# Kernel tuning notes

Hardware: AMD Instinct MI355X
Metric: run time of the kernel (lower is better)

Reference implementation:

```python
import jax, jax.numpy as jnp
import numpy as np

B, L, WD = 4096, 30, 300          # batch of news, title length, word dim
H, AD = 20, 20                    # attention heads, per-head dim
MD = H * AD                       # multi_dim = 400
E, ED = 10, 100                   # entities per news, entity dim
QD = 200                          # query_vector_dim
CAT, CD = 18, 50                  # category vocab / dim
SUB, SD = 300, 50                 # subcategory vocab / dim


def _mha(x, wq, bq, wk, bk, wv, bv):
    # x: [B, L, Din] -> [B, L, MD]; standard multi-head self-attention
    b, l, _ = x.shape
    q = (x @ wq + bq).reshape(b, l, H, AD)
    k = (x @ wk + bk).reshape(b, l, H, AD)
    v = (x @ wv + bv).reshape(b, l, H, AD)
    scores = jnp.einsum('blhd,bmhd->bhlm', q, k) / jnp.sqrt(jnp.asarray(AD, x.dtype))
    attn = jax.nn.softmax(scores, axis=-1)
    out = jnp.einsum('bhlm,bmhd->blhd', attn, v)
    return out.reshape(b, l, MD)


def _layernorm(x, g, b):
    mu = jnp.mean(x, axis=-1, keepdims=True)
    var = jnp.var(x, axis=-1, keepdims=True)
    return (x - mu) / jnp.sqrt(var + 1e-5) * g + b


def _additive(x, w, b, q):
    # x: [B, L, D] -> [B, D]
    scores = jnp.tanh(x @ w + b) @ q            # [B, L]
    alpha = jax.nn.softmax(scores, axis=-1)
    return jnp.einsum('bl,bld->bd', alpha, x)


def setup_inputs() -> dict:
    key = jax.random.key(0)
    ks = iter(jax.random.split(key, 40))
    n = lambda shape, s=0.02: (jax.random.normal(next(ks), shape, dtype=jnp.float32) * s)
    inp = {
        'word_embedding': jax.random.normal(next(ks), (B, L, WD), dtype=jnp.float32),
        'entity_embedding': jax.random.normal(next(ks), (B, E, ED), dtype=jnp.float32),
        'category_index': jax.random.randint(next(ks), (B,), 0, CAT, dtype=jnp.int64 if jax.config.jax_enable_x64 else jnp.int32),
        'subcategory_index': jax.random.randint(next(ks), (B,), 0, SUB, dtype=jnp.int64 if jax.config.jax_enable_x64 else jnp.int32),
        # category / subcategory branches
        'emb_cat': n((CAT, CD), 1.0), 'fc1_w': n((CD, MD)), 'fc1_b': jnp.zeros((MD,), jnp.float32),
        'emb_sub': n((SUB, SD), 1.0), 'fc2_w': n((SD, MD)), 'fc2_b': jnp.zeros((MD,), jnp.float32),
        # word multi-head self-attention
        'wq': n((WD, MD)), 'bq': jnp.zeros((MD,), jnp.float32),
        'wk': n((WD, MD)), 'bk': jnp.zeros((MD,), jnp.float32),
        'wv': n((WD, MD)), 'bv': jnp.zeros((MD,), jnp.float32),
        # shared LayerNorm
        'ln_g': jnp.ones((MD,), jnp.float32), 'ln_b': jnp.zeros((MD,), jnp.float32),
        # word additive attention
        'wa_w': n((MD, QD)), 'wa_b': jnp.zeros((QD,), jnp.float32), 'wa_q': n((QD,), 1.0),
        # entity branch: fc3 + GCN (learnable adjacency over the E entities of a news)
        'fc3_w': n((ED, ED)), 'fc3_b': jnp.zeros((ED,), jnp.float32),
        'gcn_A': n((E, E), 1.0), 'gcn_w': n((ED, MD)), 'gcn_b': jnp.zeros((MD,), jnp.float32),
        'ea_w': n((MD, QD)), 'ea_b': jnp.zeros((QD,), jnp.float32), 'ea_q': n((QD,), 1.0),
        # final news-level additive attention over 4 views
        'na_w': n((MD, QD)), 'na_b': jnp.zeros((QD,), jnp.float32), 'na_q': n((QD,), 1.0),
    }
    return inp


def reference(word_embedding, entity_embedding, category_index, subcategory_index,
              emb_cat, fc1_w, fc1_b, emb_sub, fc2_w, fc2_b,
              wq, bq, wk, bk, wv, bv, ln_g, ln_b,
              wa_w, wa_b, wa_q, fc3_w, fc3_b, gcn_A, gcn_w, gcn_b,
              ea_w, ea_b, ea_q, na_w, na_b, na_q):
    # category / subcategory reps (dropout is identity in eval)
    cat_rep = jnp.tanh(emb_cat[category_index] @ fc1_w + fc1_b)      # [B, MD]
    sub_rep = jnp.tanh(emb_sub[subcategory_index] @ fc2_w + fc2_b)   # [B, MD]
    # word branch
    w = _mha(word_embedding, wq, bq, wk, bk, wv, bv)                 # [B, L, MD]
    w = _layernorm(w, ln_g, ln_b)
    word_rep = jnp.tanh(_additive(w, wa_w, wa_b, wa_q))              # [B, MD]
    # entity branch: fc3 -> intra-news GCN -> shared LayerNorm
    e = jnp.tanh(entity_embedding @ fc3_w + fc3_b)                   # [B, E, ED]
    e = jax.nn.relu(jnp.einsum('ef,bfd->bed', gcn_A, e) @ gcn_w + gcn_b)  # [B, E, MD]
    e = _layernorm(e, ln_g, ln_b)
    ent_rep = jnp.tanh(_additive(e, ea_w, ea_b, ea_q))               # [B, MD]
    # fuse the 4 views with additive attention
    views = jnp.stack([word_rep, ent_rep, cat_rep, sub_rep], axis=1)  # [B, 4, MD]
    news_rep = jnp.tanh(_additive(views, na_w, na_b, na_q))          # [B, MD]
    return news_rep
```

## Files before the change

kernel.cpp:

```cpp
#include <hip/hip_runtime.h>
#include <hip/hip_bf16.h>
#include <math.h>

#define B_  4096
#define L_  30
#define WD_ 300
#define H_  20
#define AD_ 20
#define MD_ 400
#define E_  10
#define ED_ 100
#define QD_ 200
#define CD_ 50
#define SD_ 50

typedef unsigned short ushort_t;
typedef __attribute__((ext_vector_type(8))) short bf16x8_t;
typedef __attribute__((ext_vector_type(4))) float f32x4_t;

#define SX_STR   328
#define QKVQ_STR 306
#define SOB_STR  408
#define OUTB_STR 424
#define SOUT_STR 401
#define P_STR    40
#define WT_K     320
#define WAT_K    416

#define N_WT    (1200 * WT_K)
#define N_WAT   (208 * WAT_K)
#define N_FC3T  (112 * 128)
#define N_GCNT  (400 * 128)
#define N_EAT   (208 * WAT_K)

union FragU {
  unsigned  u[4];
  short     s[8];
  bf16x8_t  h;
};

__device__ __forceinline__ ushort_t f2bf(float f) {
  unsigned u = __builtin_bit_cast(unsigned, f);
  unsigned r = (u + 0x7fffu + ((u >> 16) & 1u)) >> 16;
  return (ushort_t)r;
}
__device__ __forceinline__ float bf2f(ushort_t h) {
  return __builtin_bit_cast(float, ((unsigned)h) << 16);
}
__device__ __forceinline__ float wave_reduce_sum(float v) {
  #pragma unroll
  for (int off = 32; off > 0; off >>= 1) v += __shfl_xor(v, off);
  return v;
}
__device__ __forceinline__ void split2(float v, ushort_t* __restrict__ H,
                                       ushort_t* __restrict__ Lo, int idx) {
  const ushort_t h = f2bf(v);
  H[idx] = h;
  Lo[idx] = f2bf(v - bf2f(h));
}

__global__ __launch_bounds__(256) void prep_weights(
    const float* __restrict__ wq, const float* __restrict__ wk, const float* __restrict__ wv,
    const float* __restrict__ wa_w, const float* __restrict__ fc3_w,
    const float* __restrict__ gcn_w, const float* __restrict__ ea_w,
    ushort_t* __restrict__ Wt, ushort_t* __restrict__ Wat,
    ushort_t* __restrict__ fc3TH, ushort_t* __restrict__ fc3TL,
    ushort_t* __restrict__ gcnTH, ushort_t* __restrict__ gcnTL,
    ushort_t* __restrict__ eaTH, ushort_t* __restrict__ eaTL)
{
  int idx = blockIdx.x * 256 + threadIdx.x;
  if (idx < N_WT) {
    const int n = idx / WT_K, k = idx - n * WT_K;
    float v = 0.f;
    if (k < WD_) {
      const float* w = (n < 400) ? wq : (n < 800) ? wk : wv;
      const int c = (n < 400) ? n : (n < 800) ? n - 400 : n - 800;
      v = w[k * MD_ + c];
    }
    Wt[idx] = f2bf(v);
    return;
  }
  idx -= N_WT;
  if (idx < N_WAT) {
    const int q = idx / WAT_K, d = idx - q * WAT_K;
    Wat[idx] = (q < QD_ && d < MD_) ? f2bf(wa_w[d * QD_ + q]) : (ushort_t)0;
    return;
  }
  idx -= N_WAT;
  if (idx < N_FC3T) {
    const int n = idx / 128, k = idx - n * 128;
    const float v = (n < ED_ && k < ED_) ? fc3_w[k * ED_ + n] : 0.f;
    split2(v, fc3TH, fc3TL, idx);
    return;
  }
  idx -= N_FC3T;
  if (idx < N_GCNT) {
    const int n = idx / 128, k = idx - n * 128;
    const float v = (k < ED_) ? gcn_w[k * MD_ + n] : 0.f;
    split2(v, gcnTH, gcnTL, idx);
    return;
  }
  idx -= N_GCNT;
  if (idx < N_EAT) {
    const int q = idx / WAT_K, d = idx - q * WAT_K;
    const float v = (q < QD_ && d < MD_) ? ea_w[d * QD_ + q] : 0.f;
    split2(v, eaTH, eaTL, idx);
  }
}

__global__ __launch_bounds__(512, 4) void word_branch_kernel(
    const float* __restrict__ X,
    const ushort_t* __restrict__ Wt, const ushort_t* __restrict__ Wat,
    const float* __restrict__ bq, const float* __restrict__ bk, const float* __restrict__ bv,
    const float* __restrict__ ln_g, const float* __restrict__ ln_b,
    const float* __restrict__ wa_b, const float* __restrict__ wa_q,
    float* __restrict__ word_rep)
{
  __shared__ __align__(16) ushort_t sX[32 * SX_STR];
  __shared__ __align__(16) ushort_t qkvQ[30 * QKVQ_STR];
  __shared__ __align__(16) ushort_t sOb[30 * SOB_STR];
  __shared__ __align__(16) ushort_t pT[8 * 16 * P_STR];
  __shared__ float sSc[32];
  __shared__ float sAlpha[32];

  const int b    = blockIdx.x;
  const int tid  = threadIdx.x;
  const int wave = tid >> 6;
  const int lane = tid & 63;
  const int lr   = lane & 15;
  const int kg   = lane >> 4;

  const float* xb = X + (size_t)b * (L_ * WD_);
  for (int idx = tid; idx < 32 * 320; idx += 512) {
    const int r = idx / 320, c = idx - (idx / 320) * 320;
    const float v = (r < L_ && c < WD_) ? xb[r * WD_ + c] : 0.f;
    sX[r * SX_STR + c] = f2bf(v);
  }
  for (int id = tid; id < 30 * 8; id += 512) {
    const int r = id >> 3, c = 400 + (id & 7);
    sOb[r * SOB_STR + c] = 0;
  }
  if (tid < 32) sSc[tid] = 0.f;
  __syncthreads();

  ushort_t* pw = &pT[wave * (16 * P_STR)];
  #pragma unroll 1
  for (int pass = 0; pass < 4; ++pass) {
    const int qb = (100 * pass) & ~15;
    const int p100 = 100 * pass;

    for (int t = wave; t < 21; t += 8) {
      const int sect = t / 7, ti = t - sect * 7;
      const int gq = qb + ti * 16 + lr;
      const int gcol = gq + ((sect == 0) ? 0 : (sect == 1) ? 400 : 800);
      const ushort_t* wbase = &Wt[gcol * WT_K + kg * 8];
      f32x4_t acc0 = {0,0,0,0}, acc1 = {0,0,0,0};
      #pragma unroll
      for (int ks = 0; ks < 10; ++ks) {
        bf16x8_t bf  = *reinterpret_cast<const bf16x8_t*>(wbase + ks * 32);
        bf16x8_t af0 = *reinterpret_cast<const bf16x8_t*>(&sX[lr * SX_STR + ks * 32 + kg * 8]);
        bf16x8_t af1 = *reinterpret_cast<const bf16x8_t*>(&sX[(16 + lr) * SX_STR + ks * 32 + kg * 8]);
        acc0 = __builtin_amdgcn_mfma_f32_16x16x32_bf16(af0, bf, acc0, 0, 0, 0);
        acc1 = __builtin_amdgcn_mfma_f32_16x16x32_bf16(af1, bf, acc1, 0, 0, 0);
      }
      const float bias = (gcol < 400) ? bq[gcol] : (gcol < 800) ? bk[gcol - 400] : bv[gcol - 800];
      const int lq = gq - p100;
      if (lq >= 0 && lq < 100) {
        const int lcol = sect * 102 + lq;
        #pragma unroll
        for (int i = 0; i < 4; ++i) {
          qkvQ[(kg * 4 + i) * QKVQ_STR + lcol] = f2bf(acc0[i] + bias);
          const int r2 = 16 + kg * 4 + i;
          if (r2 < L_) qkvQ[r2 * QKVQ_STR + lcol] = f2bf(acc1[i] + bias);
        }
      }
    }
    __syncthreads();

    for (int u = wave; u < 10; u += 8) {
      const int hl = u >> 1, mt = u & 1;
      const int h = pass * 5 + hl;
      const int qloc = hl * 20, kloc = 102 + hl * 20, vloc = 204 + hl * 20;

      bf16x8_t aq, bkf[2];
      {
        FragU fq;
        fq.u[0]=fq.u[1]=fq.u[2]=fq.u[3]=0;
        const bool okrow = (mt == 0) || (lr < 14);
        if (okrow && kg < 3) {
          const ushort_t* pq = &qkvQ[(mt * 16 + lr) * QKVQ_STR + qloc + kg * 8];
          fq.u[0] = *(const unsigned*)(pq);     fq.u[1] = *(const unsigned*)(pq + 2);
          if (kg < 2) { fq.u[2] = *(const unsigned*)(pq + 4); fq.u[3] = *(const unsigned*)(pq + 6); }
        }
        aq = fq.h;
      }
      #pragma unroll
      for (int t = 0; t < 2; ++t) {
        FragU fk;
        fk.u[0]=fk.u[1]=fk.u[2]=fk.u[3]=0;
        const bool okrow = (t == 0) || (lr < 14);
        if (okrow && kg < 3) {
          const ushort_t* pk = &qkvQ[(t * 16 + lr) * QKVQ_STR + kloc + kg * 8];
          fk.u[0] = *(const unsigned*)(pk);     fk.u[1] = *(const unsigned*)(pk + 2);
          if (kg < 2) { fk.u[2] = *(const unsigned*)(pk + 4); fk.u[3] = *(const unsigned*)(pk + 6); }
        }
        bkf[t] = fk.h;
      }
      f32x4_t c0 = {0,0,0,0}, c1 = {0,0,0,0};
      c0 = __builtin_amdgcn_mfma_f32_16x16x32_bf16(aq, bkf[0], c0, 0, 0, 0);
      c1 = __builtin_amdgcn_mfma_f32_16x16x32_bf16(aq, bkf[1], c1, 0, 0, 0);

      const float SCALE = 0.2236067977499790f;
      #pragma unroll
      for (int i = 0; i < 4; ++i) {
        const float v0 = c0[i] * SCALE;
        const float v1 = (lr < 14) ? c1[i] * SCALE : -1e30f;
        float mx = fmaxf(v0, v1);
        mx = fmaxf(mx, __shfl_xor(mx, 1));
        mx = fmaxf(mx, __shfl_xor(mx, 2));
        mx = fmaxf(mx, __shfl_xor(mx, 4));
        mx = fmaxf(mx, __shfl_xor(mx, 8));
        const float e0 = __expf(v0 - mx);
        const float e1 = (lr < 14) ? __expf(v1 - mx) : 0.f;
        float s = e0 + e1;
        s += __shfl_xor(s, 1);
        s += __shfl_xor(s, 2);
        s += __shfl_xor(s, 4);
        s += __shfl_xor(s, 8);
        const float inv = 1.f / s;
        const int row = kg * 4 + i;
        pw[row * P_STR + lr]      = f2bf(e0 * inv);
        pw[row * P_STR + 16 + lr] = f2bf(e1 * inv);
      }
      __asm__ volatile("s_waitcnt lgkmcnt(0)" ::: "memory");

      bf16x8_t ap = *reinterpret_cast<const bf16x8_t*>(&pw[lr * P_STR + kg * 8]);
      bf16x8_t bvf[2];
      #pragma unroll
      for (int nt = 0; nt < 2; ++nt) {
        FragU f;
        const int d = nt * 16 + lr;
        if (d < AD_) {
          #pragma unroll
          for (int j = 0; j < 8; ++j) {
            const int rm = kg * 8 + j;
            f.s[j] = (rm < L_) ? (short)qkvQ[rm * QKVQ_STR + vloc + d] : (short)0;
          }
        } else {
          f.u[0]=f.u[1]=f.u[2]=f.u[3]=0;
        }
        bvf[nt] = f.h;
      }
      f32x4_t o0 = {0,0,0,0}, o1 = {0,0,0,0};
      o0 = __builtin_amdgcn_mfma_f32_16x16x32_bf16(ap, bvf[0], o0, 0, 0, 0);
      o1 = __builtin_amdgcn_mfma_f32_16x16x32_bf16(ap, bvf[1], o1, 0, 0, 0);

      #pragma unroll
      for (int nt = 0; nt < 2; ++nt) {
        const f32x4_t o = nt ? o1 : o0;
        const int d = nt * 16 + lr;
        if (d < AD_) {
          #pragma unroll
          for (int i = 0; i < 4; ++i) {
            const int r = mt * 16 + kg * 4 + i;
            if (r < L_) sOb[r * SOB_STR + h * AD_ + d] = f2bf(o[i]);
          }
        }
      }
    }
    __syncthreads();
  }

  for (int r = wave; r < L_; r += 8) {
    float s = 0.f, s2 = 0.f;
    #pragma unroll
    for (int j = 0; j < 7; ++j) {
      const int d = lane + j * 64;
      if (d < MD_) { const float v = bf2f(sOb[r * SOB_STR + d]); s += v; s2 += v * v; }
    }
    s  = wave_reduce_sum(s);
    s2 = wave_reduce_sum(s2);
    const float mu  = s * (1.f / MD_);
    const float var = s2 * (1.f / MD_) - mu * mu;
    const float inv = rsqrtf(var + 1e-5f);
    #pragma unroll
    for (int j = 0; j < 7; ++j) {
      const int d = lane + j * 64;
      if (d < MD_) {
        const float nv = (bf2f(sOb[r * SOB_STR + d]) - mu) * inv * ln_g[d] + ln_b[d];
        sOb[r * SOB_STR + d] = f2bf(nv);
      }
    }
  }
  __syncthreads();

  for (int t = wave; t < 26; t += 8) {
    const int mt = t & 1, nt = t >> 1;
    const int row = mt * 16 + lr;
    const bool okrow = row < L_;
    const ushort_t* wbase = &Wat[(nt * 16 + lr) * WAT_K + kg * 8];
    f32x4_t acc = {0,0,0,0};
    #pragma unroll
    for (int ks = 0; ks < 13; ++ks) {
      bf16x8_t af;
      if (okrow && !(ks == 12 && kg == 3)) {
        af = *reinterpret_cast<const bf16x8_t*>(&sOb[row * SOB_STR + ks * 32 + kg * 8]);
      } else {
        FragU z; z.u[0]=z.u[1]=z.u[2]=z.u[3]=0; af = z.h;
      }
      bf16x8_t wf = *reinterpret_cast<const bf16x8_t*>(wbase + ks * 32);
      acc = __builtin_amdgcn_mfma_f32_16x16x32_bf16(af, wf, acc, 0, 0, 0);
    }
    const int q = nt * 16 + lr;
    if (q < QD_) {
      const float bb = wa_b[q], qq = wa_q[q];
      #pragma unroll
      for (int i = 0; i < 4; ++i) {
        const int rr = mt * 16 + kg * 4 + i;
        if (rr < L_) atomicAdd(&sSc[rr], tanhf(acc[i] + bb) * qq);
      }
    }
  }
  __syncthreads();

  if (wave == 0) {
    const float v = (lane < L_) ? sSc[lane] : -1e30f;
    float mx = v;
    #pragma unroll
    for (int off = 32; off > 0; off >>= 1) mx = fmaxf(mx, __shfl_xor(mx, off));
    const float e = (lane < L_) ? __expf(v - mx) : 0.f;
    float s = e;
    #pragma unroll
    for (int off = 32; off > 0; off >>= 1) s += __shfl_xor(s, off);
    if (lane < L_) sAlpha[lane] = e / s;
  }
  __syncthreads();

  if (tid < MD_) {
    const int d = tid;
    float acc = 0.f;
    #pragma unroll 6
    for (int l = 0; l < L_; ++l) acc += sAlpha[l] * bf2f(sOb[l * SOB_STR + d]);
    word_rep[(size_t)b * MD_ + d] = tanhf(acc);
  }
}

__global__ __launch_bounds__(512, 4) void entity_branch_kernel(
    const float* __restrict__ Ein,
    const ushort_t* __restrict__ fc3TH, const ushort_t* __restrict__ fc3TL,
    const float* __restrict__ fc3_b,
    const float* __restrict__ gcn_A,
    const ushort_t* __restrict__ gcnTH, const ushort_t* __restrict__ gcnTL,
    const float* __restrict__ gcn_b,
    const float* __restrict__ ln_g, const float* __restrict__ ln_b,
    const ushort_t* __restrict__ eaTH, const ushort_t* __restrict__ eaTL,
    const float* __restrict__ ea_b, const float* __restrict__ ea_q,
    float* __restrict__ ent_rep)
{
  __shared__ __align__(16) ushort_t sEh[16 * 136], sEl[16 * 136];
  __shared__ __align__(16) float    eF[E_ * 104];
  __shared__ __align__(16) ushort_t gH[16 * 136], gL[16 * 136];
  __shared__ __align__(16) float    sR[16 * SOUT_STR];
  __shared__ __align__(16) ushort_t oH[16 * OUTB_STR], oL[16 * OUTB_STR];
  __shared__ float sSc[16];
  __shared__ float sAlpha[16];

  const int b    = blockIdx.x;
  const int tid  = threadIdx.x;
  const int wave = tid >> 6;
  const int lane = tid & 63;
  const int lr   = lane & 15;
  const int kg   = lane >> 4;

  for (int id = tid; id < 16 * 128; id += 512) {
    const int r = id >> 7, c = id & 127;
    const float v = (r < E_ && c < ED_) ? Ein[(size_t)b * (E_ * ED_) + r * ED_ + c] : 0.f;
    const ushort_t hh = f2bf(v);
    sEh[r * 136 + c] = hh;
    sEl[r * 136 + c] = f2bf(v - bf2f(hh));
  }
  for (int id = tid; id < 16 * 136; id += 512) { gH[id] = 0; gL[id] = 0; }
  for (int id = tid; id < 16 * OUTB_STR; id += 512) { oH[id] = 0; oL[id] = 0; }
  if (tid < 16) sSc[tid] = 0.f;
  __syncthreads();

  for (int nt = wave; nt < 7; nt += 8) {
    f32x4_t acc = {0,0,0,0};
    #pragma unroll
    for (int ks = 0; ks < 4; ++ks) {
      const int kb = ks * 32 + kg * 8;
      bf16x8_t ah = *reinterpret_cast<const bf16x8_t*>(&sEh[lr * 136 + kb]);
      bf16x8_t al = *reinterpret_cast<const bf16x8_t*>(&sEl[lr * 136 + kb]);
      bf16x8_t wh = *reinterpret_cast<const bf16x8_t*>(&fc3TH[(nt * 16 + lr) * 128 + kb]);
      bf16x8_t wl = *reinterpret_cast<const bf16x8_t*>(&fc3TL[(nt * 16 + lr) * 128 + kb]);
      acc = __builtin_amdgcn_mfma_f32_16x16x32_bf16(ah, wh, acc, 0, 0, 0);
      acc = __builtin_amdgcn_mfma_f32_16x16x32_bf16(al, wh, acc, 0, 0, 0);
      acc = __builtin_amdgcn_mfma_f32_16x16x32_bf16(ah, wl, acc, 0, 0, 0);
    }
    const int d = nt * 16 + lr;
    if (d < ED_) {
      const float bias = fc3_b[d];
      #pragma unroll
      for (int i = 0; i < 4; ++i) {
        const int r = kg * 4 + i;
        if (r < E_) eF[r * 104 + d] = tanhf(acc[i] + bias);
      }
    }
  }
  __syncthreads();

  for (int id = tid; id < E_ * ED_; id += 512) {
    const int i = id / ED_, d = id - (id / ED_) * ED_;
    float acc = 0.f;
    #pragma unroll
    for (int f = 0; f < E_; ++f) acc += gcn_A[i * E_ + f] * eF[f * 104 + d];
    const ushort_t hh = f2bf(acc);
    gH[i * 136 + d] = hh;
    gL[i * 136 + d] = f2bf(acc - bf2f(hh));
  }
  __syncthreads();

  for (int nt = wave; nt < 25; nt += 8) {
    f32x4_t acc = {0,0,0,0};
    #pragma unroll
    for (int ks = 0; ks < 4; ++ks) {
      const int kb = ks * 32 + kg * 8;
      bf16x8_t ah = *reinterpret_cast<const bf16x8_t*>(&gH[lr * 136 + kb]);
      bf16x8_t al = *reinterpret_cast<const bf16x8_t*>(&gL[lr * 136 + kb]);
      bf16x8_t wh = *reinterpret_cast<const bf16x8_t*>(&gcnTH[(nt * 16 + lr) * 128 + kb]);
      bf16x8_t wl = *reinterpret_cast<const bf16x8_t*>(&gcnTL[(nt * 16 + lr) * 128 + kb]);
      acc = __builtin_amdgcn_mfma_f32_16x16x32_bf16(ah, wh, acc, 0, 0, 0);
      acc = __builtin_amdgcn_mfma_f32_16x16x32_bf16(al, wh, acc, 0, 0, 0);
      acc = __builtin_amdgcn_mfma_f32_16x16x32_bf16(ah, wl, acc, 0, 0, 0);
    }
    const int d = nt * 16 + lr;
    const float bias = gcn_b[d];
    #pragma unroll
    for (int i = 0; i < 4; ++i) {
      const int r = kg * 4 + i;
      if (r < E_) sR[r * SOUT_STR + d] = fmaxf(acc[i] + bias, 0.f);
    }
  }
  __syncthreads();

  for (int r = wave; r < E_; r += 8) {
    float s = 0.f, s2 = 0.f;
    for (int d = lane; d < MD_; d += 64) { const float v = sR[r * SOUT_STR + d]; s += v; s2 += v * v; }
    s  = wave_reduce_sum(s);
    s2 = wave_reduce_sum(s2);
    const float mu  = s * (1.f / MD_);
    const float var = s2 * (1.f / MD_) - mu * mu;
    const float inv = rsqrtf(var + 1e-5f);
    for (int d = lane; d < MD_; d += 64) {
      const float nv = (sR[r * SOUT_STR + d] - mu) * inv * ln_g[d] + ln_b[d];
      sR[r * SOUT_STR + d] = nv;
      const ushort_t hh = f2bf(nv);
      oH[r * OUTB_STR + d] = hh;
      oL[r * OUTB_STR + d] = f2bf(nv - bf2f(hh));
    }
  }
  __syncthreads();

  for (int nt = wave; nt < 13; nt += 8) {
    f32x4_t acc = {0,0,0,0};
    for (int ks = 0; ks < 13; ++ks) {
      const int kb = ks * 32 + kg * 8;
      bf16x8_t ah = *reinterpret_cast<const bf16x8_t*>(&oH[lr * OUTB_STR + kb]);
      bf16x8_t al = *reinterpret_cast<const bf16x8_t*>(&oL[lr * OUTB_STR + kb]);
      bf16x8_t wh = *reinterpret_cast<const bf16x8_t*>(&eaTH[(nt * 16 + lr) * WAT_K + kb]);
      bf16x8_t wl = *reinterpret_cast<const bf16x8_t*>(&eaTL[(nt * 16 + lr) * WAT_K + kb]);
      acc = __builtin_amdgcn_mfma_f32_16x16x32_bf16(ah, wh, acc, 0, 0, 0);
      acc = __builtin_amdgcn_mfma_f32_16x16x32_bf16(al, wh, acc, 0, 0, 0);
      acc = __builtin_amdgcn_mfma_f32_16x16x32_bf16(ah, wl, acc, 0, 0, 0);
    }
    const int q = nt * 16 + lr;
    if (q < QD_) {
      const float bb = ea_b[q], qq = ea_q[q];
      #pragma unroll
      for (int i = 0; i < 4; ++i) {
        const int r = kg * 4 + i;
        if (r < E_) atomicAdd(&sSc[r], tanhf(acc[i] + bb) * qq);
      }
    }
  }
  __syncthreads();

  if (wave == 0) {
    const float v = (lane < E_) ? sSc[lane] : -1e30f;
    float mx = v;
    #pragma unroll
    for (int off = 32; off > 0; off >>= 1) mx = fmaxf(mx, __shfl_xor(mx, off));
    const float e = (lane < E_) ? __expf(v - mx) : 0.f;
    float s = e;
    #pragma unroll
    for (int off = 32; off > 0; off >>= 1) s += __shfl_xor(s, off);
    if (lane < E_) sAlpha[lane] = e / s;
  }
  __syncthreads();

  if (tid < MD_) {
    const int d = tid;
    float acc = 0.f;
    #pragma unroll
    for (int i = 0; i < E_; ++i) acc += sAlpha[i] * sR[i * SOUT_STR + d];
    ent_rep[(size_t)b * MD_ + d] = tanhf(acc);
  }
}

__global__ __launch_bounds__(256) void catsub_kernel(
    const int* __restrict__ cat_idx, const int* __restrict__ sub_idx,
    const float* __restrict__ emb_cat, const float* __restrict__ fc1_w, const float* __restrict__ fc1_b,
    const float* __restrict__ emb_sub, const float* __restrict__ fc2_w, const float* __restrict__ fc2_b,
    float* __restrict__ cat_rep, float* __restrict__ sub_rep)
{
  int idx = blockIdx.x * 256 + threadIdx.x;
  const int total = B_ * MD_;
  if (idx < total) {
    const int b = idx / MD_, d = idx - (idx / MD_) * MD_;
    const float* row = emb_cat + (size_t)cat_idx[b] * CD_;
    float acc = fc1_b[d];
    #pragma unroll
    for (int k = 0; k < CD_; ++k) acc += row[k] * fc1_w[k * MD_ + d];
    cat_rep[idx] = tanhf(acc);
  } else {
    idx -= total;
    if (idx < total) {
      const int b = idx / MD_, d = idx - (idx / MD_) * MD_;
      const float* row = emb_sub + (size_t)sub_idx[b] * SD_;
      float acc = fc2_b[d];
      #pragma unroll
      for (int k = 0; k < SD_; ++k) acc += row[k] * fc2_w[k * MD_ + d];
      sub_rep[idx] = tanhf(acc);
    }
  }
}

__global__ __launch_bounds__(256) void fuse_kernel(
    const float* __restrict__ word_rep, const float* __restrict__ ent_rep,
    const float* __restrict__ cat_rep, const float* __restrict__ sub_rep,
    const float* __restrict__ na_w, const float* __restrict__ na_b, const float* __restrict__ na_q,
    float* __restrict__ out)
{
  __shared__ float sViews[4][MD_];
  __shared__ float sSc[4];
  __shared__ float sAlpha[4];
  const int b = blockIdx.x, tid = threadIdx.x;
  for (int d = tid; d < MD_; d += 256) {
    sViews[0][d] = word_rep[(size_t)b * MD_ + d];
    sViews[1][d] = ent_rep[(size_t)b * MD_ + d];
    sViews[2][d] = cat_rep[(size_t)b * MD_ + d];
    sViews[3][d] = sub_rep[(size_t)b * MD_ + d];
  }
  if (tid < 4) sSc[tid] = 0.f;
  __syncthreads();
  for (int id = tid; id < 4 * QD_; id += 256) {
    const int v = id / QD_, q = id - (id / QD_) * QD_;
    float acc = na_b[q];
    #pragma unroll 4
    for (int d = 0; d < MD_; ++d) acc += sViews[v][d] * na_w[d * QD_ + q];
    atomicAdd(&sSc[v], tanhf(acc) * na_q[q]);
  }
  __syncthreads();
  if (tid == 0) {
    float mx = -1e30f;
    for (int v = 0; v < 4; ++v) mx = fmaxf(mx, sSc[v]);
    float sum = 0.f;
    for (int v = 0; v < 4; ++v) { const float e = __expf(sSc[v] - mx); sAlpha[v] = e; sum += e; }
    const float inv = 1.f / sum;
    for (int v = 0; v < 4; ++v) sAlpha[v] *= inv;
  }
  __syncthreads();
  for (int d = tid; d < MD_; d += 256) {
    const float acc = sAlpha[0] * sViews[0][d] + sAlpha[1] * sViews[1][d] +
                      sAlpha[2] * sViews[2][d] + sAlpha[3] * sViews[3][d];
    out[(size_t)b * MD_ + d] = tanhf(acc);
  }
}

extern "C" void kernel_launch(void* const* d_in, const int* in_sizes, int n_in,
                              void* d_out, int out_size, void* d_ws, size_t ws_size,
                              hipStream_t stream) {
  const float* X        = (const float*)d_in[0];
  const float* Ein      = (const float*)d_in[1];
  const int*   cat_idx  = (const int*)d_in[2];
  const int*   sub_idx  = (const int*)d_in[3];
  const float* emb_cat  = (const float*)d_in[4];
  const float* fc1_w    = (const float*)d_in[5];
  const float* fc1_b    = (const float*)d_in[6];
  const float* emb_sub  = (const float*)d_in[7];
  const float* fc2_w    = (const float*)d_in[8];
  const float* fc2_b    = (const float*)d_in[9];
  const float* wq       = (const float*)d_in[10];
  const float* bq       = (const float*)d_in[11];
  const float* wk       = (const float*)d_in[12];
  const float* bk       = (const float*)d_in[13];
  const float* wv       = (const float*)d_in[14];
  const float* bv       = (const float*)d_in[15];
  const float* ln_g     = (const float*)d_in[16];
  const float* ln_b     = (const float*)d_in[17];
  const float* wa_w     = (const float*)d_in[18];
  const float* wa_b     = (const float*)d_in[19];
  const float* wa_q     = (const float*)d_in[20];
  const float* fc3_w    = (const float*)d_in[21];
  const float* fc3_b    = (const float*)d_in[22];
  const float* gcn_A    = (const float*)d_in[23];
  const float* gcn_w    = (const float*)d_in[24];
  const float* gcn_b    = (const float*)d_in[25];
  const float* ea_w     = (const float*)d_in[26];
  const float* ea_b     = (const float*)d_in[27];
  const float* ea_q     = (const float*)d_in[28];
  const float* na_w     = (const float*)d_in[29];
  const float* na_b     = (const float*)d_in[30];
  const float* na_q     = (const float*)d_in[31];

  float* out = (float*)d_out;
  const size_t BM = (size_t)B_ * MD_;
  float* word_rep = (float*)d_ws;
  float* ent_rep  = word_rep + BM;
  float* cat_rep  = ent_rep + BM;
  float* sub_rep  = cat_rep + BM;
  ushort_t* Wt    = (ushort_t*)(sub_rep + BM);
  ushort_t* Wat   = Wt + N_WT;
  ushort_t* fc3TH = Wat + N_WAT;
  ushort_t* fc3TL = fc3TH + N_FC3T;
  ushort_t* gcnTH = fc3TL + N_FC3T;
  ushort_t* gcnTL = gcnTH + N_GCNT;
  ushort_t* eaTH  = gcnTL + N_GCNT;
  ushort_t* eaTL  = eaTH + N_EAT;

  {
    const int total = N_WT + N_WAT + N_FC3T + N_GCNT + N_EAT;
    prep_weights<<<(total + 255) / 256, 256, 0, stream>>>(
        wq, wk, wv, wa_w, fc3_w, gcn_w, ea_w,
        Wt, Wat, fc3TH, fc3TL, gcnTH, gcnTL, eaTH, eaTL);
  }
  word_branch_kernel<<<B_, 512, 0, stream>>>(X, Wt, Wat, bq, bk, bv,
                                             ln_g, ln_b, wa_b, wa_q, word_rep);
  entity_branch_kernel<<<B_, 512, 0, stream>>>(Ein, fc3TH, fc3TL, fc3_b, gcn_A,
                                               gcnTH, gcnTL, gcn_b,
                                               ln_g, ln_b, eaTH, eaTL, ea_b, ea_q, ent_rep);
  catsub_kernel<<<(2 * B_ * MD_) / 256, 256, 0, stream>>>(cat_idx, sub_idx,
                                                          emb_cat, fc1_w, fc1_b,
                                                          emb_sub, fc2_w, fc2_b,
                                                          cat_rep, sub_rep);
  fuse_kernel<<<B_, 256, 0, stream>>>(word_rep, ent_rep, cat_rep, sub_rep,
                                      na_w, na_b, na_q, out);
}
```

Before: 1.316 ms.

## Merge word, entity and cat/sub kernels into one interleaved mega-kernel

Combines the word-branch, entity-branch and category/subcategory kernels into a single launch. Blocks alternate between word and entity work, and the cat/sub work comes last, with all three sharing one union shared-memory buffer. The aim is to cut launch gaps and tail effects and to mix the MFMA-heavy word blocks with the lighter entity blocks on each CU so they overlap. In exchange, every block reserves the largest shared-memory footprint, and the cat/sub blocks now reserve about 74KB they do not use. Register pressure is also bounded by the heavier branch, which may hurt occupancy.

```diff
diff --git a/kernel.cpp b/kernel.cpp
--- a/kernel.cpp
+++ b/kernel.cpp
@@ -32,6 +32,8 @@
 #define N_FC3T  (112 * 128)
 #define N_GCNT  (400 * 128)
 #define N_EAT   (208 * WAT_K)
+
+#define SMEM_BYTES 74496
 
 union FragU {
   unsigned  u[4];
@@ -108,7 +110,8 @@
   }
 }
 
-__global__ __launch_bounds__(512, 4) void word_branch_kernel(
+__device__ void word_body(
+    int b, char* smem,
     const float* __restrict__ X,
     const ushort_t* __restrict__ Wt, const ushort_t* __restrict__ Wat,
     const float* __restrict__ bq, const float* __restrict__ bk, const float* __restrict__ bv,
@@ -116,14 +119,13 @@
     const float* __restrict__ wa_b, const float* __restrict__ wa_q,
     float* __restrict__ word_rep)
 {
-  __shared__ __align__(16) ushort_t sX[32 * SX_STR];
-  __shared__ __align__(16) ushort_t qkvQ[30 * QKVQ_STR];
-  __shared__ __align__(16) ushort_t sOb[30 * SOB_STR];
-  __shared__ __align__(16) ushort_t pT[8 * 16 * P_STR];
-  __shared__ float sSc[32];
-  __shared__ float sAlpha[32];
-
-  const int b    = blockIdx.x;
+  ushort_t* sX     = (ushort_t*)(smem + 0);
+  ushort_t* qkvQ   = (ushort_t*)(smem + 20992);
+  ushort_t* sOb    = (ushort_t*)(smem + 39360);
+  ushort_t* pT     = (ushort_t*)(smem + 63840);
+  float*    sSc    = (float*)(smem + 74080);
+  float*    sAlpha = (float*)(smem + 74208);
+
   const int tid  = threadIdx.x;
   const int wave = tid >> 6;
   const int lane = tid & 63;
@@ -143,7 +145,7 @@
   if (tid < 32) sSc[tid] = 0.f;
   __syncthreads();
 
-  ushort_t* pw = &pT[wave * (16 * P_STR)];
+  ushort_t* pw = pT + wave * (16 * P_STR);
   #pragma unroll 1
   for (int pass = 0; pass < 4; ++pass) {
     const int qb = (100 * pass) & ~15;
@@ -345,7 +347,8 @@
   }
 }
 
-__global__ __launch_bounds__(512, 4) void entity_branch_kernel(
+__device__ void entity_body(
+    int b, char* smem,
     const float* __restrict__ Ein,
     const ushort_t* __restrict__ fc3TH, const ushort_t* __restrict__ fc3TL,
     const float* __restrict__ fc3_b,
@@ -357,15 +360,17 @@
     const float* __restrict__ ea_b, const float* __restrict__ ea_q,
     float* __restrict__ ent_rep)
 {
-  __shared__ __align__(16) ushort_t sEh[16 * 136], sEl[16 * 136];
-  __shared__ __align__(16) float    eF[E_ * 104];
-  __shared__ __align__(16) ushort_t gH[16 * 136], gL[16 * 136];
-  __shared__ __align__(16) float    sR[16 * SOUT_STR];
-  __shared__ __align__(16) ushort_t oH[16 * OUTB_STR], oL[16 * OUTB_STR];
-  __shared__ float sSc[16];
-  __shared__ float sAlpha[16];
-
-  const int b    = blockIdx.x;
+  ushort_t* sEh    = (ushort_t*)(smem + 0);
+  ushort_t* sEl    = (ushort_t*)(smem + 4352);
+  float*    eF     = (float*)(smem + 8704);
+  ushort_t* gH     = (ushort_t*)(smem + 12864);
+  ushort_t* gL     = (ushort_t*)(smem + 17216);
+  float*    sR     = (float*)(smem + 21568);
+  ushort_t* oH     = (ushort_t*)(smem + 47232);
+  ushort_t* oL     = (ushort_t*)(smem + 60800);
+  float*    sSc    = (float*)(smem + 74368);
+  float*    sAlpha = (float*)(smem + 74432);
+
   const int tid  = threadIdx.x;
   const int wave = tid >> 6;
   const int lane = tid & 63;
@@ -507,30 +512,57 @@
   }
 }
 
-__global__ __launch_bounds__(256) void catsub_kernel(
+__global__ __launch_bounds__(512, 4) void mega_kernel(
+    const float* __restrict__ X,
+    const ushort_t* __restrict__ Wt, const ushort_t* __restrict__ Wat,
+    const float* __restrict__ bq, const float* __restrict__ bk, const float* __restrict__ bv,
+    const float* __restrict__ ln_g, const float* __restrict__ ln_b,
+    const float* __restrict__ wa_b, const float* __restrict__ wa_q,
+    float* __restrict__ word_rep,
+    const float* __restrict__ Ein,
+    const ushort_t* __restrict__ fc3TH, const ushort_t* __restrict__ fc3TL,
+    const float* __restrict__ fc3_b,
+    const float* __restrict__ gcn_A,
+    const ushort_t* __restrict__ gcnTH, const ushort_t* __restrict__ gcnTL,
+    const float* __restrict__ gcn_b,
+    const ushort_t* __restrict__ eaTH, const ushort_t* __restrict__ eaTL,
+    const float* __restrict__ ea_b, const float* __restrict__ ea_q,
+    float* __restrict__ ent_rep,
     const int* __restrict__ cat_idx, const int* __restrict__ sub_idx,
     const float* __restrict__ emb_cat, const float* __restrict__ fc1_w, const float* __restrict__ fc1_b,
     const float* __restrict__ emb_sub, const float* __restrict__ fc2_w, const float* __restrict__ fc2_b,
     float* __restrict__ cat_rep, float* __restrict__ sub_rep)
 {
-  int idx = blockIdx.x * 256 + threadIdx.x;
-  const int total = B_ * MD_;
-  if (idx < total) {
-    const int b = idx / MD_, d = idx - (idx / MD_) * MD_;
-    const float* row = emb_cat + (size_t)cat_idx[b] * CD_;
-    float acc = fc1_b[d];
-    #pragma unroll
-    for (int k = 0; k < CD_; ++k) acc += row[k] * fc1_w[k * MD_ + d];
-    cat_rep[idx] = tanhf(acc);
+  __shared__ __align__(16) char smem[SMEM_BYTES];
+  const int bid = blockIdx.x;
+  if (bid < 2 * B_) {
+    if ((bid & 1) == 0) {
+      word_body(bid >> 1, smem, X, Wt, Wat, bq, bk, bv, ln_g, ln_b,
+                wa_b, wa_q, word_rep);
+    } else {
+      entity_body(bid >> 1, smem, Ein, fc3TH, fc3TL, fc3_b, gcn_A,
+                  gcnTH, gcnTL, gcn_b, ln_g, ln_b, eaTH, eaTL, ea_b, ea_q, ent_rep);
+    }
   } else {
-    idx -= total;
+    int idx = (bid - 2 * B_) * 512 + threadIdx.x;
+    const int total = B_ * MD_;
     if (idx < total) {
       const int b = idx / MD_, d = idx - (idx / MD_) * MD_;
-      const float* row = emb_sub + (size_t)sub_idx[b] * SD_;
-      float acc = fc2_b[d];
-      #pragma unroll
-      for (int k = 0; k < SD_; ++k) acc += row[k] * fc2_w[k * MD_ + d];
-      sub_rep[idx] = tanhf(acc);
+      const float* row = emb_cat + (size_t)cat_idx[b] * CD_;
+      float acc = fc1_b[d];
+      #pragma unroll
+      for (int k = 0; k < CD_; ++k) acc += row[k] * fc1_w[k * MD_ + d];
+      cat_rep[idx] = tanhf(acc);
+    } else {
+      idx -= total;
+      if (idx < total) {
+        const int b = idx / MD_, d = idx - (idx / MD_) * MD_;
+        const float* row = emb_sub + (size_t)sub_idx[b] * SD_;
+        float acc = fc2_b[d];
+        #pragma unroll
+        for (int k = 0; k < SD_; ++k) acc += row[k] * fc2_w[k * MD_ + d];
+        sub_rep[idx] = tanhf(acc);
+      }
     }
   }
 }
@@ -634,15 +666,16 @@
         wq, wk, wv, wa_w, fc3_w, gcn_w, ea_w,
         Wt, Wat, fc3TH, fc3TL, gcnTH, gcnTL, eaTH, eaTL);
   }
-  word_branch_kernel<<<B_, 512, 0, stream>>>(X, Wt, Wat, bq, bk, bv,
-                                             ln_g, ln_b, wa_b, wa_q, word_rep);
-  entity_branch_kernel<<<B_, 512, 0, stream>>>(Ein, fc3TH, fc3TL, fc3_b, gcn_A,
-                                               gcnTH, gcnTL, gcn_b,
-                                               ln_g, ln_b, eaTH, eaTL, ea_b, ea_q, ent_rep);
-  catsub_kernel<<<(2 * B_ * MD_) / 256, 256, 0, stream>>>(cat_idx, sub_idx,
-                                                          emb_cat, fc1_w, fc1_b,
-                                                          emb_sub, fc2_w, fc2_b,
-                                                          cat_rep, sub_rep);
+  {
+    const int catsubBlocks = (2 * B_ * MD_) / 512;
+    const int megaBlocks = 2 * B_ + catsubBlocks;
+    mega_kernel<<<megaBlocks, 512, 0, stream>>>(
+        X, Wt, Wat, bq, bk, bv, ln_g, ln_b, wa_b, wa_q, word_rep,
+        Ein, fc3TH, fc3TL, fc3_b, gcn_A, gcnTH, gcnTL, gcn_b,
+        eaTH, eaTL, ea_b, ea_q, ent_rep,
+        cat_idx, sub_idx, emb_cat, fc1_w, fc1_b, emb_sub, fc2_w, fc2_b,
+        cat_rep, sub_rep);
+  }
   fuse_kernel<<<B_, 256, 0, stream>>>(word_rep, ent_rep, cat_rep, sub_rep,
                                       na_w, na_b, na_q, out);
 }
```

Result: slower. 1.776 ms (+34.9%).
